# Performance work log

Hardware: AMD Instinct MI355X
Metric: run time of the kernel (lower is better)

Reference implementation:

```python
import jax, jax.numpy as jnp
import numpy as np
from jax import lax

ALPHA = 50.0
BN_EPS = 1e-5
L2_EPS = 1e-12

N, C, H, W = 32, 128, 128, 128
K = 64  # num_clusters


def _l2norm(v, axis):
    n = jnp.sqrt(jnp.sum(v * v, axis=axis, keepdims=True))
    return v / jnp.maximum(n, L2_EPS)


def setup_inputs() -> dict:
    key = jax.random.key(0)
    ks = jax.random.split(key, 4)
    x = jax.random.normal(ks[0], (N, C, H, W), dtype=jnp.float32)
    conv_w = jax.random.normal(ks[1], (C, C, 3, 3), dtype=jnp.float32) * 0.05
    bn_gamma = jnp.ones((C,), jnp.float32)
    bn_beta = jnp.zeros((C,), jnp.float32)
    bn_mean = jnp.zeros((C,), jnp.float32)
    bn_var = jnp.ones((C,), jnp.float32)
    # conv.weight in NetVLAD is centroids.permute(1,0): shape (dim, num_clusters)
    vlad_w = jax.random.normal(ks[2], (C, K), dtype=jnp.float32)
    vlad_b = jnp.zeros((K,), jnp.float32)  # initialized to zeros in _init_params
    return {"input": x, "conv_w": conv_w, "bn_gamma": bn_gamma, "bn_beta": bn_beta,
            "bn_mean": bn_mean, "bn_var": bn_var, "vlad_w": vlad_w, "vlad_b": vlad_b,
            "norm_flag": 1}


def reference(input, conv_w, bn_gamma, bn_beta, bn_mean, bn_var, vlad_w, vlad_b, norm_flag):
    # bottleneck_layer_2: conv3x3 stride2 pad1 (no bias) -> BN (eval form) -> ReLU
    f = lax.conv_general_dilated(input, conv_w, window_strides=(2, 2),
                                 padding=[(1, 1), (1, 1)],
                                 dimension_numbers=("NCHW", "OIHW", "NCHW"))
    inv = bn_gamma / jnp.sqrt(bn_var + BN_EPS)
    f = f * inv[None, :, None, None] + (bn_beta - bn_mean * inv)[None, :, None, None]
    f = jax.nn.relu(f)

    n, c, h, w = f.shape
    hw = h * w
    # normalize_input: L2 over channel dim
    xn = _l2norm(f, axis=1)
    xf = xn.reshape(n, c, hw)  # (N,C,HW)

    # soft assignment: x^T @ normalize(W, dim=0), bias added, softmax over clusters
    wn = _l2norm(vlad_w, axis=0)                     # (C,K)
    sa_ = jnp.einsum("nci,ck->nik", xf, wn)          # (N,HW,K)
    logits = jnp.swapaxes(sa_, 1, 2) + vlad_b[None, :, None]  # (N,K,HW)
    a = jax.nn.softmax(ALPHA * logits, axis=1)       # softmax over K

    # vlad_k = sum_i a_ki * x_i - (sum_i a_ki) * c_k  (c_k = vlad_w[:,k], unnormalized)
    asum = jnp.sum(a, axis=-1)                       # (N,K)
    vlad = jnp.einsum("nki,nci->nkc", a, xf) - asum[:, :, None] * vlad_w.T[None]  # (N,K,C)

    vlad = _l2norm(vlad, axis=2)                     # intra-normalization
    vlad = vlad.reshape(n, -1)
    vlad = _l2norm(vlad, axis=1)

    feature = jnp.swapaxes(xf, 1, 2)                 # (N,HW,C)
    soft_assign_out = jnp.swapaxes(sa_, 1, 2)        # (N,K,HW)
    return (vlad, soft_assign_out, feature)
```

## Files before the change

kernel.cpp:

```cpp
#include <hip/hip_runtime.h>

typedef short short8 __attribute__((ext_vector_type(8)));
typedef float floatx4 __attribute__((ext_vector_type(4)));

#define ALPHA 50.0f
#define BN_EPS 1e-5f

#define SA_BASE   262144L
#define FEAT_BASE 8650752L

#define T_OFF    0L
#define WB_OFF   138444800L
#define WNA_OFF  138739712L
#define ASUM_OFF 138756096L
#define VACC_OFF 138764288L

__device__ __forceinline__ unsigned short f2bf(float f) {
    unsigned u = __builtin_bit_cast(unsigned, f);
    u = u + 0x7FFFu + ((u >> 16) & 1u);
    return (unsigned short)(u >> 16);
}

__device__ __forceinline__ void gl_lds16(const void* g, void* l) {
    __builtin_amdgcn_global_load_lds(
        (const __attribute__((address_space(1))) unsigned int*)g,
        (__attribute__((address_space(3))) unsigned int*)l, 16, 0, 0);
}

__global__ __launch_bounds__(256) void k_prep(const float* __restrict__ conv_w,
                                              const float* __restrict__ vlad_w,
                                              unsigned short* __restrict__ wB,
                                              unsigned short* __restrict__ wnA) {
    int b = blockIdx.x, t = threadIdx.x;
    if (b < 576) {
        int idx = b * 256 + t;
        int ci = idx & 127, co = (idx >> 7) & 127, tap = idx >> 14;
        float w = conv_w[(co * 128 + ci) * 9 + tap];
        wB[(tap * 128 + co) * 128 + ci] = f2bf(w);
    } else if (t < 64) {
        int k = t;
        float s = 0.0f;
        for (int c = 0; c < 128; c++) { float w = vlad_w[c * 64 + k]; s += w * w; }
        float rs = 1.0f / fmaxf(sqrtf(s), 1e-12f);
        for (int c = 0; c < 128; c++) wnA[k * 128 + c] = f2bf(vlad_w[c * 64 + k] * rs);
    }
}

__global__ __launch_bounds__(256) void k_border(unsigned short* __restrict__ T,
                                                float* __restrict__ vacc,
                                                float* __restrict__ asum) {
    int n = blockIdx.x, t = threadIdx.x;
    uint4 z = make_uint4(0, 0, 0, 0);
    for (int i = t; i < 4128; i += 256) {
        long e;
        if (i < 2080) {
            int ix = i >> 4, oct = i & 15;
            e = (((long)n * 130 + 0) * 130 + ix) * 128 + oct * 8;
        } else {
            int j = i - 2080;
            int row = (j >> 4) + 1, oct = j & 15;
            e = (((long)n * 130 + row) * 130 + 0) * 128 + oct * 8;
        }
        *(uint4*)(T + e) = z;
    }
    float4 zf = make_float4(0.f, 0.f, 0.f, 0.f);
    for (int i = t; i < 2048; i += 256)
        *(float4*)(vacc + (long)n * 8192 + i * 4) = zf;
    if (t < 64) asum[n * 64 + t] = 0.0f;
}

__global__ __launch_bounds__(256) void k_xform(const float* __restrict__ in,
                                               unsigned short* __restrict__ T) {
    int y = blockIdx.x, n = blockIdx.y, t = threadIdx.x;
    __shared__ float ls[64 * 133];
    for (int cc = 0; cc < 2; cc++) {
        __syncthreads();
        int ci0 = cc * 64;
#pragma unroll
        for (int i = 0; i < 8; i++) {
            int idx = i * 256 + t;
            int ci = idx >> 5, xq = idx & 31;
            float4 v = *(const float4*)(in + ((((long)n * 128 + ci0 + ci) * 128 + y) * 128 + xq * 4));
            *(float4*)(&ls[ci * 133 + xq * 4]) = v;
        }
        __syncthreads();
#pragma unroll
        for (int i = 0; i < 4; i++) {
            int idx = i * 256 + t;
            int x = idx >> 3, oct = idx & 7;
            short8 pk;
#pragma unroll
            for (int j = 0; j < 8; j++)
                pk[j] = (short)f2bf(ls[(oct * 8 + j) * 133 + x]);
            long e = (((long)n * 130 + y + 1) * 130 + (x + 1)) * 128 + ci0 + oct * 8;
            *(short8*)(T + e) = pk;
        }
    }
}

__global__ __launch_bounds__(256) void k_conv(const unsigned short* __restrict__ T,
                                              const unsigned short* __restrict__ wB,
                                              const float* __restrict__ gamma,
                                              const float* __restrict__ beta,
                                              const float* __restrict__ mean,
                                              const float* __restrict__ var,
                                              const unsigned short* __restrict__ wnA,
                                              const float* __restrict__ vlad_b,
                                              float* __restrict__ out,
                                              float* __restrict__ vacc,
                                              float* __restrict__ asum) {
    int y = blockIdx.x, n = blockIdx.y;
    int t = threadIdx.x, lane = t & 63, w = t >> 6;
    int wm = w >> 1, wn = w & 1;
    int s = lane & 15, q = lane >> 4;

    __shared__ __align__(16) short lsA[13824];
    __shared__ float lsq[256];

    floatx4 acc[2][4];
#pragma unroll
    for (int a = 0; a < 2; a++)
#pragma unroll
        for (int b = 0; b < 4; b++) acc[a][b] = (floatx4){0.f, 0.f, 0.f, 0.f};

    const unsigned short* Tbase = T + (((long)n * 130 + 2 * y) * 130) * 128;
    int bbase0 = (wn * 64 + s) * 128 + q * 8;

    for (int cc = 0; cc < 4; cc++) {
        int ci0 = cc * 32;
        const unsigned short* Tc = Tbase + ci0;
#pragma unroll
        for (int i = 0; i < 7; i++) {
            int f = i * 256 + t;
            short* lbase = &lsA[2048 * i + 512 * w];
            if (f < 1560) {
                int r = f / 520;
                int rem = f - r * 520;
                int p = rem >> 3;
                int o8 = (rem & 7) ^ (p & 7);
                int ix = 2 * p + (o8 >> 2);
                int oct = o8 & 3;
                gl_lds16(Tc + (((long)(r * 130 + ix)) << 7) + (oct << 3), lbase);
            }
        }
        __syncthreads();
#pragma unroll
        for (int tap = 0; tap < 9; tap++) {
            const int dy = tap / 3, dx = tap % 3;
            short8 af[2], bf[4];
#pragma unroll
            for (int tm = 0; tm < 2; tm++) {
                int x = wm * 32 + tm * 16 + s;
                int p = x + (dx >> 1);
                int o8p = (((dx & 1) << 2) | q) ^ (p & 7);
                af[tm] = *(const short8*)(&lsA[(((dy * 65 + p) << 3) + o8p) << 3]);
            }
#pragma unroll
            for (int tn = 0; tn < 4; tn++)
                bf[tn] = *(const short8*)(wB + bbase0 + tap * 16384 + tn * 2048 + ci0);
#pragma unroll
            for (int tm = 0; tm < 2; tm++)
#pragma unroll
                for (int tn = 0; tn < 4; tn++)
                    acc[tm][tn] = __builtin_amdgcn_mfma_f32_16x16x32_bf16(af[tm], bf[tn], acc[tm][tn], 0, 0, 0);
        }
        __syncthreads();
    }

    float inv[4], bt[4];
#pragma unroll
    for (int tn = 0; tn < 4; tn++) {
        int co = wn * 64 + tn * 16 + s;
        inv[tn] = gamma[co] / sqrtf(var[co] + BN_EPS);
        bt[tn] = beta[co] - mean[co] * inv[tn];
    }
#pragma unroll
    for (int tm = 0; tm < 2; tm++)
#pragma unroll
        for (int tn = 0; tn < 4; tn++)
#pragma unroll
            for (int r = 0; r < 4; r++) {
                float f = acc[tm][tn][r] * inv[tn] + bt[tn];
                acc[tm][tn][r] = fmaxf(f, 0.0f);
            }
#pragma unroll
    for (int tm = 0; tm < 2; tm++)
#pragma unroll
        for (int r = 0; r < 4; r++) {
            float p = 0.f;
#pragma unroll
            for (int tn = 0; tn < 4; tn++) { float f = acc[tm][tn][r]; p += f * f; }
            p += __shfl_xor(p, 1); p += __shfl_xor(p, 2);
            p += __shfl_xor(p, 4); p += __shfl_xor(p, 8);
            if (s == 0) lsq[wn * 64 + wm * 32 + tm * 16 + q * 4 + r] = p;
        }
    __syncthreads();
    float scl[2][4];
#pragma unroll
    for (int tm = 0; tm < 2; tm++)
#pragma unroll
        for (int r = 0; r < 4; r++) {
            int m = wm * 32 + tm * 16 + q * 4 + r;
            float tot = lsq[m] + lsq[64 + m];
            scl[tm][r] = 1.0f / fmaxf(sqrtf(tot), 1e-12f);
        }
    short* lsT = lsA;
    long pixbase = (long)n * 4096 + y * 64;
#pragma unroll
    for (int tm = 0; tm < 2; tm++)
#pragma unroll
        for (int r = 0; r < 4; r++) {
            int m = wm * 32 + tm * 16 + q * 4 + r;
#pragma unroll
            for (int tn = 0; tn < 4; tn++) {
                int co = wn * 64 + tn * 16 + s;
                float xv = acc[tm][tn][r] * scl[tm][r];
                out[FEAT_BASE + (pixbase + m) * 128 + co] = xv;
                lsT[co * 72 + m] = (short)f2bf(xv);
            }
        }
    __syncthreads();

    floatx4 acc2[4];
#pragma unroll
    for (int a = 0; a < 4; a++) acc2[a] = (floatx4){0.f, 0.f, 0.f, 0.f};
    int pixw = w * 16;
#pragma unroll
    for (int kk = 0; kk < 4; kk++) {
        int c0 = kk * 32 + q * 8;
        short8 af2[4], bf2;
#pragma unroll
        for (int tm = 0; tm < 4; tm++)
            af2[tm] = *(const short8*)(wnA + (tm * 16 + s) * 128 + c0);
#pragma unroll
        for (int j = 0; j < 8; j++)
            bf2[j] = lsT[(c0 + j) * 72 + pixw + s];
#pragma unroll
        for (int tm = 0; tm < 4; tm++)
            acc2[tm] = __builtin_amdgcn_mfma_f32_16x16x32_bf16(af2[tm], bf2, acc2[tm], 0, 0, 0);
    }
    long sabase = SA_BASE + (long)n * 262144 + y * 64 + pixw;
#pragma unroll
    for (int tm = 0; tm < 4; tm++)
#pragma unroll
        for (int r = 0; r < 4; r++) {
            int k = tm * 16 + q * 4 + r;
            out[sabase + (long)k * 4096 + s] = acc2[tm][r];
        }
    float bv2[4][4];
#pragma unroll
    for (int tm = 0; tm < 4; tm++)
#pragma unroll
        for (int r = 0; r < 4; r++) bv2[tm][r] = vlad_b[tm * 16 + q * 4 + r];
    float M = -1e30f;
#pragma unroll
    for (int tm = 0; tm < 4; tm++)
#pragma unroll
        for (int r = 0; r < 4; r++)
            M = fmaxf(M, ALPHA * (acc2[tm][r] + bv2[tm][r]));
    M = fmaxf(M, __shfl_xor(M, 16)); M = fmaxf(M, __shfl_xor(M, 32));
    float S = 0.f;
#pragma unroll
    for (int tm = 0; tm < 4; tm++)
#pragma unroll
        for (int r = 0; r < 4; r++) {
            float p = expf(ALPHA * (acc2[tm][r] + bv2[tm][r]) - M);
            acc2[tm][r] = p; S += p;
        }
    S += __shfl_xor(S, 16); S += __shfl_xor(S, 32);
    float rS = 1.0f / S;
#pragma unroll
    for (int tm = 0; tm < 4; tm++)
#pragma unroll
        for (int r = 0; r < 4; r++) acc2[tm][r] *= rS;
    short* lsAa = lsA + 9216;
#pragma unroll
    for (int tm = 0; tm < 4; tm++)
#pragma unroll
        for (int r = 0; r < 4; r++) {
            int k = tm * 16 + q * 4 + r;
            lsAa[k * 72 + pixw + s] = (short)f2bf(acc2[tm][r]);
            float p = acc2[tm][r];
            p += __shfl_xor(p, 1); p += __shfl_xor(p, 2);
            p += __shfl_xor(p, 4); p += __shfl_xor(p, 8);
            if (s == 0) lsq[w * 64 + k] = p;
        }
    __syncthreads();
    if (t < 64) {
        float s4 = lsq[t] + lsq[64 + t] + lsq[128 + t] + lsq[192 + t];
        atomicAdd(asum + n * 64 + t, s4);
    }
    floatx4 acc3[2][4];
#pragma unroll
    for (int a = 0; a < 2; a++)
#pragma unroll
        for (int b = 0; b < 4; b++) acc3[a][b] = (floatx4){0.f, 0.f, 0.f, 0.f};
    int kh = (w >> 1) * 32, ch0 = (w & 1) * 64;
#pragma unroll
    for (int pc = 0; pc < 2; pc++) {
        int p0 = pc * 32 + q * 8;
        short8 aA[2], bB[4];
#pragma unroll
        for (int tk = 0; tk < 2; tk++)
            aA[tk] = *(const short8*)(lsAa + (kh + tk * 16 + s) * 72 + p0);
#pragma unroll
        for (int tc = 0; tc < 4; tc++)
            bB[tc] = *(const short8*)(lsT + (ch0 + tc * 16 + s) * 72 + p0);
#pragma unroll
        for (int tk = 0; tk < 2; tk++)
#pragma unroll
            for (int tc = 0; tc < 4; tc++)
                acc3[tk][tc] = __builtin_amdgcn_mfma_f32_16x16x32_bf16(aA[tk], bB[tc], acc3[tk][tc], 0, 0, 0);
    }
    float* vb = vacc + (long)n * 8192;
#pragma unroll
    for (int tk = 0; tk < 2; tk++)
#pragma unroll
        for (int r = 0; r < 4; r++) {
            int k = kh + tk * 16 + q * 4 + r;
#pragma unroll
            for (int tc = 0; tc < 4; tc++)
                atomicAdd(vb + k * 128 + ch0 + tc * 16 + s, acc3[tk][tc][r]);
        }
}

__global__ __launch_bounds__(256) void k_vlad2(const float* __restrict__ vacc,
                                               const float* __restrict__ vlad_w,
                                               const float* __restrict__ asum,
                                               float* __restrict__ out) {
    int n = blockIdx.x;
    int t = threadIdx.x, lane = t & 63, w = t >> 6;
    __shared__ float lsq[128];
    __shared__ float gsq[4];

    float v[32];
    const float* vb = vacc + (long)n * 8192;
#pragma unroll
    for (int j = 0; j < 32; j++) {
        int e = j * 256 + t;
        int k = e >> 7, c = e & 127;
        float sacc = vb[e] - asum[n * 64 + k] * vlad_w[c * 64 + k];
        v[j] = sacc;
        float p = sacc * sacc;
        p += __shfl_xor(p, 1); p += __shfl_xor(p, 2); p += __shfl_xor(p, 4);
        p += __shfl_xor(p, 8); p += __shfl_xor(p, 16); p += __shfl_xor(p, 32);
        if (lane == 0) lsq[j * 4 + w] = p;
    }
    __syncthreads();
    float gp = 0.f;
#pragma unroll
    for (int j = 0; j < 32; j++) {
        float tot = lsq[j * 4 + (w & 2)] + lsq[j * 4 + (w & 2) + 1];
        float sc = 1.0f / fmaxf(sqrtf(tot), 1e-12f);
        v[j] *= sc;
        gp += v[j] * v[j];
    }
    gp += __shfl_xor(gp, 1); gp += __shfl_xor(gp, 2); gp += __shfl_xor(gp, 4);
    gp += __shfl_xor(gp, 8); gp += __shfl_xor(gp, 16); gp += __shfl_xor(gp, 32);
    if (lane == 0) gsq[w] = gp;
    __syncthreads();
    float sc2 = 1.0f / fmaxf(sqrtf(gsq[0] + gsq[1] + gsq[2] + gsq[3]), 1e-12f);
#pragma unroll
    for (int j = 0; j < 32; j++)
        out[(long)n * 8192 + j * 256 + t] = v[j] * sc2;
}

extern "C" void kernel_launch(void* const* d_in, const int* in_sizes, int n_in,
                              void* d_out, int out_size, void* d_ws, size_t ws_size,
                              hipStream_t stream) {
    const float* input  = (const float*)d_in[0];
    const float* conv_w = (const float*)d_in[1];
    const float* gamma  = (const float*)d_in[2];
    const float* beta   = (const float*)d_in[3];
    const float* mean   = (const float*)d_in[4];
    const float* var    = (const float*)d_in[5];
    const float* vlad_w = (const float*)d_in[6];
    const float* vlad_b = (const float*)d_in[7];
    float* out = (float*)d_out;
    char* ws = (char*)d_ws;

    unsigned short* T   = (unsigned short*)(ws + T_OFF);
    unsigned short* wB  = (unsigned short*)(ws + WB_OFF);
    unsigned short* wnA = (unsigned short*)(ws + WNA_OFF);
    float* asum         = (float*)(ws + ASUM_OFF);
    float* vacc         = (float*)(ws + VACC_OFF);

    k_prep<<<577, 256, 0, stream>>>(conv_w, vlad_w, wB, wnA);
    k_border<<<32, 256, 0, stream>>>(T, vacc, asum);
    k_xform<<<dim3(128, 32), 256, 0, stream>>>(input, T);
    k_conv<<<dim3(64, 32), 256, 0, stream>>>(T, wB, gamma, beta, mean, var, wnA, vlad_b, out, vacc, asum);
    k_vlad2<<<32, 256, 0, stream>>>(vacc, vlad_w, asum, out);
}
```

Before: 632.8 us.

## Double-buffer conv input staging and split VLAD aggregation into deterministic partial reductions

The conv kernel now stages channel chunks into two LDS buffers, using manual waitcnt and barriers so global-to-LDS loads overlap MFMA compute. The VLAD accumulation moves out of the conv kernel. A new kernel rereads the stored features and soft assignments, writes per-row partial sums instead of global atomics, and two further kernels reduce the partials and normalize. This removes atomic contention and lowers LDS and register pressure in the conv kernel. In exchange it adds extra global traffic (bf16 assignment buffer, fp32 feature reread, 64 partial 8192-float slices per image) and two more launches.

Measured after the change: 652.8 us. 3.2% more time.

```diff
diff --git a/kernel.cpp b/kernel.cpp
--- a/kernel.cpp
+++ b/kernel.cpp
@@ -9,11 +9,14 @@
 #define SA_BASE   262144L
 #define FEAT_BASE 8650752L
 
-#define T_OFF    0L
-#define WB_OFF   138444800L
-#define WNA_OFF  138739712L
-#define ASUM_OFF 138756096L
-#define VACC_OFF 138764288L
+#define PART_OFF  0L
+#define T_OFF     0L
+#define WB_OFF    138444800L
+#define WNA_OFF   138739712L
+#define AW_OFF    138756096L
+#define ASUMP_OFF 155533312L
+#define VTMP_OFF  156057600L
+#define GPART_OFF 157106176L
 
 __device__ __forceinline__ unsigned short f2bf(float f) {
     unsigned u = __builtin_bit_cast(unsigned, f);
@@ -46,9 +49,7 @@
     }
 }
 
-__global__ __launch_bounds__(256) void k_border(unsigned short* __restrict__ T,
-                                                float* __restrict__ vacc,
-                                                float* __restrict__ asum) {
+__global__ __launch_bounds__(256) void k_border(unsigned short* __restrict__ T) {
     int n = blockIdx.x, t = threadIdx.x;
     uint4 z = make_uint4(0, 0, 0, 0);
     for (int i = t; i < 4128; i += 256) {
@@ -63,10 +64,6 @@
         }
         *(uint4*)(T + e) = z;
     }
-    float4 zf = make_float4(0.f, 0.f, 0.f, 0.f);
-    for (int i = t; i < 2048; i += 256)
-        *(float4*)(vacc + (long)n * 8192 + i * 4) = zf;
-    if (t < 64) asum[n * 64 + t] = 0.0f;
 }
 
 __global__ __launch_bounds__(256) void k_xform(const float* __restrict__ in,
@@ -107,15 +104,15 @@
                                               const unsigned short* __restrict__ wnA,
                                               const float* __restrict__ vlad_b,
                                               float* __restrict__ out,
-                                              float* __restrict__ vacc,
-                                              float* __restrict__ asum) {
+                                              unsigned short* __restrict__ aw) {
     int y = blockIdx.x, n = blockIdx.y;
     int t = threadIdx.x, lane = t & 63, w = t >> 6;
     int wm = w >> 1, wn = w & 1;
     int s = lane & 15, q = lane >> 4;
 
-    __shared__ __align__(16) short lsA[13824];
-    __shared__ float lsq[256];
+    __shared__ __align__(16) short bufA[12480];
+    __shared__ __align__(16) short bufB[12480];
+    __shared__ float lsq[128];
 
     floatx4 acc[2][4];
 #pragma unroll
@@ -126,13 +123,12 @@
     const unsigned short* Tbase = T + (((long)n * 130 + 2 * y) * 130) * 128;
     int bbase0 = (wn * 64 + s) * 128 + q * 8;
 
-    for (int cc = 0; cc < 4; cc++) {
-        int ci0 = cc * 32;
-        const unsigned short* Tc = Tbase + ci0;
+    auto STAGE = [&](short* dst, int cc) {
+        const unsigned short* Tc = Tbase + cc * 32;
 #pragma unroll
         for (int i = 0; i < 7; i++) {
             int f = i * 256 + t;
-            short* lbase = &lsA[2048 * i + 512 * w];
+            short* lbase = dst + 2048 * i + 512 * w;
             if (f < 1560) {
                 int r = f / 520;
                 int rem = f - r * 520;
@@ -143,7 +139,9 @@
                 gl_lds16(Tc + (((long)(r * 130 + ix)) << 7) + (oct << 3), lbase);
             }
         }
-        __syncthreads();
+    };
+    auto COMPUTE = [&](const short* sb, int cc) {
+        int ci0 = cc * 32;
 #pragma unroll
         for (int tap = 0; tap < 9; tap++) {
             const int dy = tap / 3, dx = tap % 3;
@@ -153,7 +151,7 @@
                 int x = wm * 32 + tm * 16 + s;
                 int p = x + (dx >> 1);
                 int o8p = (((dx & 1) << 2) | q) ^ (p & 7);
-                af[tm] = *(const short8*)(&lsA[(((dy * 65 + p) << 3) + o8p) << 3]);
+                af[tm] = *(const short8*)(&sb[(((dy * 65 + p) << 3) + o8p) << 3]);
             }
 #pragma unroll
             for (int tn = 0; tn < 4; tn++)
@@ -164,8 +162,23 @@
                 for (int tn = 0; tn < 4; tn++)
                     acc[tm][tn] = __builtin_amdgcn_mfma_f32_16x16x32_bf16(af[tm], bf[tn], acc[tm][tn], 0, 0, 0);
         }
-        __syncthreads();
-    }
+    };
+
+    STAGE(bufA, 0);
+    STAGE(bufB, 1);
+    asm volatile("s_waitcnt vmcnt(6)\n\ts_barrier" ::: "memory");
+    COMPUTE(bufA, 0);
+    asm volatile("s_barrier" ::: "memory");
+    STAGE(bufA, 2);
+    asm volatile("s_waitcnt vmcnt(6)\n\ts_barrier" ::: "memory");
+    COMPUTE(bufB, 1);
+    asm volatile("s_barrier" ::: "memory");
+    STAGE(bufB, 3);
+    asm volatile("s_waitcnt vmcnt(6)\n\ts_barrier" ::: "memory");
+    COMPUTE(bufA, 2);
+    asm volatile("s_barrier" ::: "memory");
+    asm volatile("s_waitcnt vmcnt(0)\n\ts_barrier" ::: "memory");
+    COMPUTE(bufB, 3);
 
     float inv[4], bt[4];
 #pragma unroll
@@ -204,7 +217,7 @@
             float tot = lsq[m] + lsq[64 + m];
             scl[tm][r] = 1.0f / fmaxf(sqrtf(tot), 1e-12f);
         }
-    short* lsT = lsA;
+    short* lsT = bufA;
     long pixbase = (long)n * 4096 + y * 64;
 #pragma unroll
     for (int tm = 0; tm < 2; tm++)
@@ -269,26 +282,58 @@
         }
     S += __shfl_xor(S, 16); S += __shfl_xor(S, 32);
     float rS = 1.0f / S;
+    long awbase = ((long)n * 64) * 4096 + y * 64 + pixw + s;
 #pragma unroll
     for (int tm = 0; tm < 4; tm++)
 #pragma unroll
-        for (int r = 0; r < 4; r++) acc2[tm][r] *= rS;
-    short* lsAa = lsA + 9216;
-#pragma unroll
-    for (int tm = 0; tm < 4; tm++)
-#pragma unroll
         for (int r = 0; r < 4; r++) {
             int k = tm * 16 + q * 4 + r;
-            lsAa[k * 72 + pixw + s] = (short)f2bf(acc2[tm][r]);
-            float p = acc2[tm][r];
-            p += __shfl_xor(p, 1); p += __shfl_xor(p, 2);
-            p += __shfl_xor(p, 4); p += __shfl_xor(p, 8);
-            if (s == 0) lsq[w * 64 + k] = p;
-        }
+            aw[awbase + (long)k * 4096] = f2bf(acc2[tm][r] * rS);
+        }
+}
+
+__global__ __launch_bounds__(256) void k_vlad1(const unsigned short* __restrict__ aw,
+                                               const float* __restrict__ feat,
+                                               float* __restrict__ part,
+                                               float* __restrict__ asumP) {
+    int y = blockIdx.x, n = blockIdx.y;
+    int t = threadIdx.x, lane = t & 63, w = t >> 6;
+    int s = lane & 15, q = lane >> 4;
+
+    __shared__ __align__(16) short lsX[128 * 72];
+    __shared__ __align__(16) short lsAa[64 * 72];
+
+    {
+        int k = t >> 2, seg = t & 3;
+        const unsigned short* src = aw + ((long)n * 64 + k) * 4096 + y * 64 + seg * 16;
+        short8 v0 = *(const short8*)(src);
+        short8 v1 = *(const short8*)(src + 8);
+        *(short8*)(&lsAa[k * 72 + seg * 16]) = v0;
+        *(short8*)(&lsAa[k * 72 + seg * 16 + 8]) = v1;
+    }
+    {
+        int pix = t >> 2, cs = t & 3;
+        const float* src = feat + FEAT_BASE + ((long)n * 4096 + y * 64 + pix) * 128 + cs * 32;
+#pragma unroll
+        for (int f4 = 0; f4 < 8; f4++) {
+            float4 v = *(const float4*)(src + f4 * 4);
+            int c = cs * 32 + f4 * 4;
+            lsX[(c + 0) * 72 + pix] = (short)f2bf(v.x);
+            lsX[(c + 1) * 72 + pix] = (short)f2bf(v.y);
+            lsX[(c + 2) * 72 + pix] = (short)f2bf(v.z);
+            lsX[(c + 3) * 72 + pix] = (short)f2bf(v.w);
+        }
+    }
     __syncthreads();
     if (t < 64) {
-        float s4 = lsq[t] + lsq[64 + t] + lsq[128 + t] + lsq[192 + t];
-        atomicAdd(asum + n * 64 + t, s4);
+        float sacc = 0.f;
+#pragma unroll
+        for (int p = 0; p < 64; p++) {
+            unsigned short u = (unsigned short)lsAa[t * 72 + p];
+            unsigned ui = ((unsigned)u) << 16;
+            sacc += __builtin_bit_cast(float, ui);
+        }
+        asumP[((long)n * 64 + y) * 64 + t] = sacc;
     }
     floatx4 acc3[2][4];
 #pragma unroll
@@ -302,17 +347,17 @@
         short8 aA[2], bB[4];
 #pragma unroll
         for (int tk = 0; tk < 2; tk++)
-            aA[tk] = *(const short8*)(lsAa + (kh + tk * 16 + s) * 72 + p0);
+            aA[tk] = *(const short8*)(&lsAa[(kh + tk * 16 + s) * 72 + p0]);
 #pragma unroll
         for (int tc = 0; tc < 4; tc++)
-            bB[tc] = *(const short8*)(lsT + (ch0 + tc * 16 + s) * 72 + p0);
+            bB[tc] = *(const short8*)(&lsX[(ch0 + tc * 16 + s) * 72 + p0]);
 #pragma unroll
         for (int tk = 0; tk < 2; tk++)
 #pragma unroll
             for (int tc = 0; tc < 4; tc++)
                 acc3[tk][tc] = __builtin_amdgcn_mfma_f32_16x16x32_bf16(aA[tk], bB[tc], acc3[tk][tc], 0, 0, 0);
     }
-    float* vb = vacc + (long)n * 8192;
+    float* pp = part + ((long)n * 64 + y) * 8192;
 #pragma unroll
     for (int tk = 0; tk < 2; tk++)
 #pragma unroll
@@ -320,49 +365,88 @@
             int k = kh + tk * 16 + q * 4 + r;
 #pragma unroll
             for (int tc = 0; tc < 4; tc++)
-                atomicAdd(vb + k * 128 + ch0 + tc * 16 + s, acc3[tk][tc][r]);
-        }
-}
-
-__global__ __launch_bounds__(256) void k_vlad2(const float* __restrict__ vacc,
-                                               const float* __restrict__ vlad_w,
-                                               const float* __restrict__ asum,
-                                               float* __restrict__ out) {
-    int n = blockIdx.x;
+                pp[k * 128 + ch0 + tc * 16 + s] = acc3[tk][tc][r];
+        }
+}
+
+__global__ __launch_bounds__(256) void k_vred(const float* __restrict__ part,
+                                              const float* __restrict__ vlad_w,
+                                              const float* __restrict__ asumP,
+                                              float* __restrict__ vtmp,
+                                              float* __restrict__ gpart) {
+    int sub = blockIdx.x, n = blockIdx.y;
     int t = threadIdx.x, lane = t & 63, w = t >> 6;
-    __shared__ float lsq[128];
-    __shared__ float gsq[4];
-
-    float v[32];
-    const float* vb = vacc + (long)n * 8192;
-#pragma unroll
-    for (int j = 0; j < 32; j++) {
-        int e = j * 256 + t;
+    __shared__ float asumT[64];
+    __shared__ float asumL[8];
+    __shared__ float lsq[16];
+    __shared__ float gred[4];
+
+    if (t < 64) {
+        int kl = t & 7, i0 = t >> 3;
+        int k = sub * 8 + kl;
+        float sacc = 0.f;
+#pragma unroll
+        for (int i = 0; i < 8; i++) sacc += asumP[((long)n * 64 + i0 + i * 8) * 64 + k];
+        asumT[t] = sacc;
+    }
+    __syncthreads();
+    if (t < 8) {
+        float sacc = 0.f;
+#pragma unroll
+        for (int g = 0; g < 8; g++) sacc += asumT[g * 8 + t];
+        asumL[t] = sacc;
+    }
+    __syncthreads();
+
+    int e0 = sub * 1024;
+    float v[4];
+    const float* pb = part + (long)n * 64 * 8192;
+#pragma unroll
+    for (int jj = 0; jj < 4; jj++) {
+        int e = e0 + jj * 256 + t;
+        float sacc = 0.f;
+#pragma unroll 8
+        for (int c8 = 0; c8 < 64; c8++) sacc += pb[c8 * 8192 + e];
         int k = e >> 7, c = e & 127;
-        float sacc = vb[e] - asum[n * 64 + k] * vlad_w[c * 64 + k];
-        v[j] = sacc;
+        sacc -= asumL[k - sub * 8] * vlad_w[c * 64 + k];
+        v[jj] = sacc;
         float p = sacc * sacc;
         p += __shfl_xor(p, 1); p += __shfl_xor(p, 2); p += __shfl_xor(p, 4);
         p += __shfl_xor(p, 8); p += __shfl_xor(p, 16); p += __shfl_xor(p, 32);
-        if (lane == 0) lsq[j * 4 + w] = p;
+        if (lane == 0) lsq[jj * 4 + w] = p;
     }
     __syncthreads();
     float gp = 0.f;
 #pragma unroll
-    for (int j = 0; j < 32; j++) {
-        float tot = lsq[j * 4 + (w & 2)] + lsq[j * 4 + (w & 2) + 1];
+    for (int jj = 0; jj < 4; jj++) {
+        float tot = lsq[jj * 4 + (w & 2)] + lsq[jj * 4 + (w & 2) + 1];
         float sc = 1.0f / fmaxf(sqrtf(tot), 1e-12f);
-        v[j] *= sc;
-        gp += v[j] * v[j];
+        v[jj] *= sc;
+        gp += v[jj] * v[jj];
+        vtmp[(long)n * 8192 + e0 + jj * 256 + t] = v[jj];
     }
     gp += __shfl_xor(gp, 1); gp += __shfl_xor(gp, 2); gp += __shfl_xor(gp, 4);
     gp += __shfl_xor(gp, 8); gp += __shfl_xor(gp, 16); gp += __shfl_xor(gp, 32);
-    if (lane == 0) gsq[w] = gp;
-    __syncthreads();
-    float sc2 = 1.0f / fmaxf(sqrtf(gsq[0] + gsq[1] + gsq[2] + gsq[3]), 1e-12f);
-#pragma unroll
-    for (int j = 0; j < 32; j++)
-        out[(long)n * 8192 + j * 256 + t] = v[j] * sc2;
+    if (lane == 0) gred[w] = gp;
+    __syncthreads();
+    if (t == 0) gpart[n * 8 + sub] = gred[0] + gred[1] + gred[2] + gred[3];
+}
+
+__global__ __launch_bounds__(256) void k_vfin(const float* __restrict__ vtmp,
+                                              const float* __restrict__ gpart,
+                                              float* __restrict__ out) {
+    int n = blockIdx.x, t = threadIdx.x;
+    __shared__ float sc2s;
+    if (t == 0) {
+        float s = 0.f;
+#pragma unroll
+        for (int i = 0; i < 8; i++) s += gpart[n * 8 + i];
+        sc2s = 1.0f / fmaxf(sqrtf(s), 1e-12f);
+    }
+    __syncthreads();
+    float sc2 = sc2s;
+    for (int i = t; i < 8192; i += 256)
+        out[(long)n * 8192 + i] = vtmp[(long)n * 8192 + i] * sc2;
 }
 
 extern "C" void kernel_launch(void* const* d_in, const int* in_sizes, int n_in,
@@ -380,14 +464,19 @@
     char* ws = (char*)d_ws;
 
     unsigned short* T   = (unsigned short*)(ws + T_OFF);
+    float* part         = (float*)(ws + PART_OFF);
     unsigned short* wB  = (unsigned short*)(ws + WB_OFF);
     unsigned short* wnA = (unsigned short*)(ws + WNA_OFF);
-    float* asum         = (float*)(ws + ASUM_OFF);
-    float* vacc         = (float*)(ws + VACC_OFF);
+    unsigned short* aw  = (unsigned short*)(ws + AW_OFF);
+    float* asumP        = (float*)(ws + ASUMP_OFF);
+    float* vtmp         = (float*)(ws + VTMP_OFF);
+    float* gpart        = (float*)(ws + GPART_OFF);
 
     k_prep<<<577, 256, 0, stream>>>(conv_w, vlad_w, wB, wnA);
-    k_border<<<32, 256, 0, stream>>>(T, vacc, asum);
+    k_border<<<32, 256, 0, stream>>>(T);
     k_xform<<<dim3(128, 32), 256, 0, stream>>>(input, T);
-    k_conv<<<dim3(64, 32), 256, 0, stream>>>(T, wB, gamma, beta, mean, var, wnA, vlad_b, out, vacc, asum);
-    k_vlad2<<<32, 256, 0, stream>>>(vacc, vlad_w, asum, out);
-}
+    k_conv<<<dim3(64, 32), 256, 0, stream>>>(T, wB, gamma, beta, mean, var, wnA, vlad_b, out, aw);
+    k_vlad1<<<dim3(64, 32), 256, 0, stream>>>(aw, out, part, asumP);
+    k_vred<<<dim3(8, 32), 256, 0, stream>>>(part, vlad_w, asumP, vtmp, gpart);
+    k_vfin<<<32, 256, 0, stream>>>(vtmp, gpart, out);
+}
```
